# Kernel tuning notes

Measured on AMD Instinct MI355X. Metric: run time of the kernel, lower is better.

The kernel has to match this reference:

```python
import jax, jax.numpy as jnp
import numpy as np
import math

D_MODEL = 768
N_HEADS = 12
D_K = 64
D_V = 64
NEG = -1e9


def setup_inputs() -> dict:
    key = jax.random.key(0)
    ks = jax.random.split(key, 12)
    bz, L = 8, 1024
    q = jax.random.normal(ks[0], (bz, L, D_MODEL), dtype=jnp.float32)
    k = jax.random.normal(ks[1], (bz, L, D_MODEL), dtype=jnp.float32)
    v = jax.random.normal(ks[2], (bz, L, D_MODEL), dtype=jnp.float32)
    att_mask = jax.random.randint(ks[3], (bz, L), 0, 2).astype(bool)  # True = padded
    # Linear weights stored as [in, out] (torch stores [out, in]; math y = x @ W + b)
    std_qk = math.sqrt(2.0 / (D_MODEL + D_K))
    std_v = math.sqrt(2.0 / (D_MODEL + D_V))
    Wq = jax.random.normal(ks[4], (D_MODEL, D_K * N_HEADS), dtype=jnp.float32) * std_qk
    Wk = jax.random.normal(ks[5], (D_MODEL, D_K * N_HEADS), dtype=jnp.float32) * std_qk
    Wv = jax.random.normal(ks[6], (D_MODEL, D_V * N_HEADS), dtype=jnp.float32) * std_v
    xav = math.sqrt(2.0 / (D_V * N_HEADS + D_MODEL))
    Wo = jax.random.normal(ks[7], (D_V * N_HEADS, D_MODEL), dtype=jnp.float32) * xav
    bq = jnp.zeros((D_K * N_HEADS,), jnp.float32)
    bk = jnp.zeros((D_K * N_HEADS,), jnp.float32)
    bv = jnp.zeros((D_V * N_HEADS,), jnp.float32)
    bo = jnp.zeros((D_MODEL,), jnp.float32)
    gamma = jnp.ones((D_MODEL,), jnp.float32)
    beta = jnp.zeros((D_MODEL,), jnp.float32)
    return {"q": q, "k": k, "v": v, "att_mask": att_mask,
            "Wq": Wq, "bq": bq, "Wk": Wk, "bk": bk, "Wv": Wv, "bv": bv,
            "Wo": Wo, "bo": bo, "gamma": gamma, "beta": beta}


def reference(q, k, v, att_mask, Wq, bq, Wk, bk, Wv, bv, Wo, bo, gamma, beta):
    bz, Lq, _ = q.shape
    Lk = k.shape[1]
    scale = 1.0 / math.sqrt(D_K)
    residual = q
    # [bz, H, L, d]
    qf = (q @ Wq + bq).reshape(bz, Lq, N_HEADS, D_K).transpose(0, 2, 1, 3)
    kf = (k @ Wk + bk).reshape(bz, Lk, N_HEADS, D_K).transpose(0, 2, 1, 3)
    vf = (v @ Wv + bv).reshape(bz, Lk, N_HEADS, D_V).transpose(0, 2, 1, 3)
    scores = jnp.einsum('bhqd,bhkd->bhqk', qf, kf) * scale
    # padding mask: True positions set to -1e9 (masked_fill semantics)
    scores = jnp.where(att_mask[:, None, None, :], NEG, scores)
    iq = jnp.arange(Lq)[:, None]
    ik = jnp.arange(Lk)[None, :]
    fw = scores + jnp.where(ik < iq, NEG, 0.0).astype(scores.dtype)  # attend diag & above
    bw = scores + jnp.where(ik > iq, NEG, 0.0).astype(scores.dtype)  # attend diag & below
    a_fw = jax.nn.softmax(fw, axis=-1)
    a_bw = jax.nn.softmax(bw, axis=-1)
    att = jnp.einsum('bhqk,bhkd->bhqd', a_fw, vf) + jnp.einsum('bhqk,bhkd->bhqd', a_bw, vf)
    att = att.transpose(0, 2, 1, 3).reshape(bz, Lq, N_HEADS * D_V)
    mh = att @ Wo + bo
    x = residual + mh
    mu = jnp.mean(x, axis=-1, keepdims=True)
    var = jnp.mean(jnp.square(x - mu), axis=-1, keepdims=True)
    return (x - mu) / jnp.sqrt(var + 1e-6) * gamma + beta
```

## Files before the change

kernel.cpp:

```cpp
#include <hip/hip_runtime.h>
#include <hip/hip_bf16.h>

typedef unsigned short u16;
typedef unsigned int u32;
typedef unsigned long long u64;
typedef __attribute__((ext_vector_type(8))) short short8v;
typedef __attribute__((ext_vector_type(4))) float f32x4;

#define MFMA16(a,b,c) __builtin_amdgcn_mfma_f32_16x16x32_bf16(a,b,c,0,0,0)
#define NEGV -1e9f
#define MOFF 20.0f

__device__ __forceinline__ float b2f(u16 u){ return __uint_as_float(((u32)u)<<16); }
__device__ __forceinline__ u16 f2b(float f){
  __hip_bfloat16 h = __float2bfloat16(f);
  return __builtin_bit_cast(u16, h);
}
__device__ __forceinline__ u32 pk2(float a, float b){
  return (u32)f2b(a) | ((u32)f2b(b) << 16);
}

__global__ __launch_bounds__(256) void wcvt(
    const float* __restrict__ W0, const float* __restrict__ W1,
    const float* __restrict__ W2, const float* __restrict__ W3,
    u16* __restrict__ Wt)
{
  __shared__ u16 Tl[64*72];
  const int z = blockIdx.z;
  const float* W = z==0 ? W0 : z==1 ? W1 : z==2 ? W2 : W3;
  u16* Wo = Wt + (size_t)z * 768 * 768;
  const int t = threadIdx.x;
  const int n0 = blockIdx.x*64, k0 = blockIdx.y*64;
  const int r = t>>2, cs = (t&3)*16;
  {
    const float* src = W + (size_t)(k0+r)*768 + n0 + cs;
    float4 f0 = ((const float4*)src)[0];
    float4 f1 = ((const float4*)src)[1];
    float4 f2 = ((const float4*)src)[2];
    float4 f3 = ((const float4*)src)[3];
    uint4 o0 = { pk2(f0.x,f0.y), pk2(f0.z,f0.w), pk2(f1.x,f1.y), pk2(f1.z,f1.w) };
    uint4 o1 = { pk2(f2.x,f2.y), pk2(f2.z,f2.w), pk2(f3.x,f3.y), pk2(f3.z,f3.w) };
    *(uint4*)&Tl[r*72 + cs]     = o0;
    *(uint4*)&Tl[r*72 + cs + 8] = o1;
  }
  __syncthreads();
  {
    u16 v[16];
    #pragma unroll
    for (int j = 0; j < 16; ++j) v[j] = Tl[(cs+j)*72 + r];
    uint4 o0, o1;
    u32* p0 = (u32*)&o0; u32* p1 = (u32*)&o1;
    #pragma unroll
    for (int j = 0; j < 4; ++j) p0[j] = (u32)v[2*j] | ((u32)v[2*j+1]<<16);
    #pragma unroll
    for (int j = 0; j < 4; ++j) p1[j] = (u32)v[8+2*j] | ((u32)v[8+2*j+1]<<16);
    *(uint4*)(Wo + (size_t)(n0+r)*768 + k0 + cs)     = o0;
    *(uint4*)(Wo + (size_t)(n0+r)*768 + k0 + cs + 8) = o1;
  }
}

template<int ABF16, int OMODE>
__global__ __launch_bounds__(256) void gemm_mfma(
    const void* __restrict__ Av, const u16* __restrict__ Wt,
    const float* __restrict__ bias, float* __restrict__ outF,
    u16* __restrict__ outB)
{
  __shared__ u16 Al[128*40];
  __shared__ u16 Bl[128*40];
  const int t = threadIdx.x;
  const int lane = t & 63, wid = t >> 6;
  const int l15 = lane & 15, lg = lane >> 4;
  const int wm = wid >> 1, wn = wid & 1;

  const int id = blockIdx.x;
  const int xcd = id & 7, rr = id >> 3;
  const int nb = rr % 6, mb = (rr / 6) * 8 + xcd;
  const int n0 = nb * 128, m0 = mb * 128;

  f32x4 acc[4][4];
  #pragma unroll
  for (int mi = 0; mi < 4; ++mi)
    #pragma unroll
    for (int ni = 0; ni < 4; ++ni)
      acc[mi][ni] = (f32x4){0.f,0.f,0.f,0.f};

  const int arow = t >> 1, aseg = (t & 1) * 16;

  for (int k0 = 0; k0 < 768; k0 += 32) {
    __syncthreads();
    if (ABF16) {
      const u16* A = (const u16*)Av + (size_t)(m0 + arow) * 768 + k0 + aseg;
      uint4 a0 = ((const uint4*)A)[0];
      uint4 a1 = ((const uint4*)A)[1];
      *(uint4*)&Al[arow*40 + aseg]     = a0;
      *(uint4*)&Al[arow*40 + aseg + 8] = a1;
    } else {
      const float* A = (const float*)Av + (size_t)(m0 + arow) * 768 + k0 + aseg;
      float4 f0 = ((const float4*)A)[0];
      float4 f1 = ((const float4*)A)[1];
      float4 f2 = ((const float4*)A)[2];
      float4 f3 = ((const float4*)A)[3];
      uint4 o0 = { pk2(f0.x,f0.y), pk2(f0.z,f0.w), pk2(f1.x,f1.y), pk2(f1.z,f1.w) };
      uint4 o1 = { pk2(f2.x,f2.y), pk2(f2.z,f2.w), pk2(f3.x,f3.y), pk2(f3.z,f3.w) };
      *(uint4*)&Al[arow*40 + aseg]     = o0;
      *(uint4*)&Al[arow*40 + aseg + 8] = o1;
    }
    {
      const u16* B = Wt + (size_t)(n0 + arow) * 768 + k0 + aseg;
      uint4 b0 = ((const uint4*)B)[0];
      uint4 b1 = ((const uint4*)B)[1];
      *(uint4*)&Bl[arow*40 + aseg]     = b0;
      *(uint4*)&Bl[arow*40 + aseg + 8] = b1;
    }
    __syncthreads();
    short8v af[4], bf[4];
    #pragma unroll
    for (int mi = 0; mi < 4; ++mi)
      af[mi] = *(const short8v*)&Al[(wm*64 + mi*16 + l15)*40 + lg*8];
    #pragma unroll
    for (int ni = 0; ni < 4; ++ni)
      bf[ni] = *(const short8v*)&Bl[(wn*64 + ni*16 + l15)*40 + lg*8];
    #pragma unroll
    for (int mi = 0; mi < 4; ++mi)
      #pragma unroll
      for (int ni = 0; ni < 4; ++ni)
        acc[mi][ni] = MFMA16(af[mi], bf[ni], acc[mi][ni]);
  }

  #pragma unroll
  for (int mi = 0; mi < 4; ++mi)
  #pragma unroll
  for (int ni = 0; ni < 4; ++ni) {
    const int col  = n0 + wn*64 + ni*16 + l15;
    const int row0 = m0 + wm*64 + mi*16 + lg*4;
    const float bv = bias[col];
    if (OMODE == 0) {
      #pragma unroll
      for (int r = 0; r < 4; ++r)
        outF[(size_t)(row0 + r) * 768 + col] = acc[mi][ni][r] + bv;
    } else if (OMODE == 1) {
      const int h = col >> 6, d = col & 63;
      #pragma unroll
      for (int r = 0; r < 4; ++r) {
        const int row = row0 + r;
        const int bb = row >> 10, l = row & 1023;
        outB[(((size_t)(bb*12 + h))*1024 + l)*64 + d] = f2b(acc[mi][ni][r] + bv);
      }
    } else {
      const int h = col >> 6, d = col & 63;
      const int bb = row0 >> 10, l0 = row0 & 1023;
      const int pos = (l0 & ~63) + ((l0 >> 5) & 1) * 32
                    + ((l0 >> 2) & 3) * 8 + ((l0 >> 4) & 1) * 4;
      ushort4 pk;
      pk.x = f2b(acc[mi][ni][0] + bv);
      pk.y = f2b(acc[mi][ni][1] + bv);
      pk.z = f2b(acc[mi][ni][2] + bv);
      pk.w = f2b(acc[mi][ni][3] + bv);
      *(ushort4*)(outB + (((size_t)(bb*12 + h))*64 + d)*1024 + pos) = pk;
    }
  }
}

template<int R>
__device__ __forceinline__ void slow_fix(
    int side, int b, int bh, int rowg0, int lane, int l15, int lg,
    const u16* __restrict__ Vs, const int* __restrict__ mask,
    float* spb, f32x4 (&acc)[4], float (&L)[4])
{
  u64 bal = __ballot(l15 == 0 && L[R] == 0.f);
  while (bal) {
    const int pos = __ffsll((unsigned long long)bal) - 1;
    bal &= bal - 1;
    const int lgi = pos >> 4;
    const int q = rowg0 + lgi*4 + R;
    const u16* vp = Vs + ((size_t)bh*64 + lane)*1024;
    const int* mp = mask + b*1024;
    float vsum = 0.f, cnt = 0.f;
    for (int m0 = 0; m0 < 1024; m0 += 8) {
      uint4 vv = *(const uint4*)(vp + m0);
      const u16* ve = (const u16*)&vv;
      const int kb = (m0 & ~63) + ((m0 >> 5) & 1) * 32 + ((m0 >> 3) & 3) * 4;
      #pragma unroll
      for (int j = 0; j < 4; ++j) {
        const int k0 = kb + j, k1 = kb + 16 + j;
        const bool a0 = side ? (k0 <= q) : (k0 >= q);
        const bool a1 = side ? (k1 <= q) : (k1 >= q);
        const float w0 = a0 ? (mp[k0] ? 1.f : 0.f) : (mp[k0] ? 0.f : 1.f);
        const float w1 = a1 ? (mp[k1] ? 1.f : 0.f) : (mp[k1] ? 0.f : 1.f);
        vsum += w0 * b2f(ve[j]) + w1 * b2f(ve[4+j]);
        cnt  += w0 + w1;
      }
    }
    spb[lane] = vsum;
    if (lg == lgi) {
      #pragma unroll
      for (int fd = 0; fd < 4; ++fd)
        acc[fd][R] = spb[fd*16 + l15];
      L[R] = cnt;
    }
  }
}

__global__ __launch_bounds__(256, 4) void attn_mfma(
    const u16* __restrict__ Qf, const u16* __restrict__ Kf,
    const u16* __restrict__ Vs, const int* __restrict__ mask,
    u16* __restrict__ att)
{
  __shared__ u16 KV[2][2][4096];
  __shared__ float spb[4][64];

  const int t = threadIdx.x;
  const int lane = t & 63, wid = t >> 6;
  const int l15 = lane & 15, lg = lane >> 4;

  const int x = blockIdx.x;
  const int xcd = x & 7, rest = x >> 3;
  const int qt = rest & 15, bhh = rest >> 4;
  const int bh = (bhh << 3) | xcd;
  const int b = bh / 12, h = bh - b*12;
  const int rowg0 = qt*64 + wid*16;
  const int qglob = rowg0 + l15;

  short8v qb0, qb1;
  {
    const u16* Qp = Qf + ((size_t)bh*1024 + rowg0 + l15)*64 + lg*8;
    qb0 = *(const short8v*)(Qp);
    qb1 = *(const short8v*)(Qp + 32);
  }

  f32x4 accf[4], accb[4];
  #pragma unroll
  for (int i = 0; i < 4; ++i) { accf[i] = (f32x4){0,0,0,0}; accb[i] = (f32x4){0,0,0,0}; }
  float Lf = 0.f, Lb = 0.f;

  const u16* Kbh = Kf + (size_t)bh*1024*64;
  const u16* Vbh = Vs + (size_t)bh*64*1024;
  const int* mbp = mask + b*1024;

  const int srow = t >> 2;
  const int sc   = (t & 3) * 2;
  const int wo0  = srow*64 + ((sc     ^ (srow & 7)) * 8);
  const int wo1  = srow*64 + (((sc+1) ^ (srow & 7)) * 8);
  const size_t kgo = (size_t)srow*64   + sc*8;
  const size_t vgo = (size_t)srow*1024 + sc*8;

  uint4 kA = *(const uint4*)(Kbh + kgo);
  uint4 kB = *(const uint4*)(Kbh + kgo + 8);
  uint4 vA = *(const uint4*)(Vbh + vgo);
  uint4 vB = *(const uint4*)(Vbh + vgo + 8);
  *(uint4*)(&KV[0][0][wo0]) = kA;
  *(uint4*)(&KV[0][0][wo1]) = kB;
  *(uint4*)(&KV[0][1][wo0]) = vA;
  *(uint4*)(&KV[0][1][wo1]) = vB;
  __syncthreads();

  int buf = 0;
  for (int kt = 0; kt < 16; ++kt) {
    if (kt < 15) {
      kA = *(const uint4*)(Kbh + (size_t)(kt+1)*64*64 + kgo);
      kB = *(const uint4*)(Kbh + (size_t)(kt+1)*64*64 + kgo + 8);
      vA = *(const uint4*)(Vbh + (size_t)(kt+1)*64 + vgo);
      vB = *(const uint4*)(Vbh + (size_t)(kt+1)*64 + vgo + 8);
    }

    const u16* KB = KV[buf][0];
    const u16* VB = KV[buf][1];

    f32x4 sv[4];
    #pragma unroll
    for (int ni = 0; ni < 4; ++ni) {
      const int krow = ni*16 + l15;
      const int s0 = (lg ^ (l15 & 7)) * 8;
      short8v ka0 = *(const short8v*)(KB + krow*64 + s0);
      short8v ka1 = *(const short8v*)(KB + krow*64 + (s0 ^ 32));
      f32x4 z = (f32x4){0,0,0,0};
      z = MFMA16(ka0, qb0, z);
      z = MFMA16(ka1, qb1, z);
      int4 pm = *(const int4*)(mbp + kt*64 + ni*16 + lg*4);
      z[0] = pm.x ? NEGV : z[0]*0.125f;
      z[1] = pm.y ? NEGV : z[1]*0.125f;
      z[2] = pm.z ? NEGV : z[2]*0.125f;
      z[3] = pm.w ? NEGV : z[3]*0.125f;
      sv[ni] = z;
    }
    const bool dg = (kt == qt);

    #pragma unroll
    for (int side = 0; side < 2; ++side) {
      if (side == 0 && kt < qt) continue;
      if (side == 1 && kt > qt) continue;
      float p[4][4];
      float Ladd = 0.f;
      #pragma unroll
      for (int ni = 0; ni < 4; ++ni)
        #pragma unroll
        for (int r = 0; r < 4; ++r) {
          float arg = sv[ni][r];
          if (dg) {
            const int key = kt*64 + ni*16 + lg*4 + r;
            const bool msk = side ? (key > qglob) : (key < qglob);
            if (msk) arg += NEGV;
          }
          const float pe = __expf(arg - MOFF);
          p[ni][r] = pe;
          Ladd += pe;
        }
      if (side == 0) Lf += Ladd; else Lb += Ladd;
      f32x4* acc = side ? accb : accf;
      #pragma unroll
      for (int a = 0; a < 2; ++a) {
        uint4 pw;
        pw.x = pk2(p[2*a][0],   p[2*a][1]);
        pw.y = pk2(p[2*a][2],   p[2*a][3]);
        pw.z = pk2(p[2*a+1][0], p[2*a+1][1]);
        pw.w = pk2(p[2*a+1][2], p[2*a+1][3]);
        short8v pa = __builtin_bit_cast(short8v, pw);
        #pragma unroll
        for (int fd = 0; fd < 4; ++fd) {
          const int vrow = fd*16 + l15;
          const int vs2 = ((a*4 + lg) ^ (l15 & 7)) * 8;
          short8v vb = *(const short8v*)(VB + vrow*64 + vs2);
          acc[fd] = MFMA16(pa, vb, acc[fd]);
        }
      }
    }

    if (kt < 15) {
      *(uint4*)(&KV[buf^1][0][wo0]) = kA;
      *(uint4*)(&KV[buf^1][0][wo1]) = kB;
      *(uint4*)(&KV[buf^1][1][wo0]) = vA;
      *(uint4*)(&KV[buf^1][1][wo1]) = vB;
    }
    __syncthreads();
    buf ^= 1;
  }

  Lf += __shfl_xor(Lf, 16); Lf += __shfl_xor(Lf, 32);
  Lb += __shfl_xor(Lb, 16); Lb += __shfl_xor(Lb, 32);
  float Lfr[4], Lbr[4];
  #pragma unroll
  for (int r = 0; r < 4; ++r) {
    const int src = (lg << 4) | (lg*4 + r);
    Lfr[r] = __shfl(Lf, src);
    Lbr[r] = __shfl(Lb, src);
  }

  float* sp = spb[wid];
  slow_fix<0>(0, b, bh, rowg0, lane, l15, lg, Vs, mask, sp, accf, Lfr);
  slow_fix<1>(0, b, bh, rowg0, lane, l15, lg, Vs, mask, sp, accf, Lfr);
  slow_fix<2>(0, b, bh, rowg0, lane, l15, lg, Vs, mask, sp, accf, Lfr);
  slow_fix<3>(0, b, bh, rowg0, lane, l15, lg, Vs, mask, sp, accf, Lfr);
  slow_fix<0>(1, b, bh, rowg0, lane, l15, lg, Vs, mask, sp, accb, Lbr);
  slow_fix<1>(1, b, bh, rowg0, lane, l15, lg, Vs, mask, sp, accb, Lbr);
  slow_fix<2>(1, b, bh, rowg0, lane, l15, lg, Vs, mask, sp, accb, Lbr);
  slow_fix<3>(1, b, bh, rowg0, lane, l15, lg, Vs, mask, sp, accb, Lbr);

  float rf[4], rb[4];
  #pragma unroll
  for (int r = 0; r < 4; ++r) { rf[r] = 1.f/Lfr[r]; rb[r] = 1.f/Lbr[r]; }
  #pragma unroll
  for (int fd = 0; fd < 4; ++fd)
    #pragma unroll
    for (int r = 0; r < 4; ++r) {
      const float val = accf[fd][r]*rf[r] + accb[fd][r]*rb[r];
      att[((size_t)(b*1024 + rowg0 + lg*4 + r))*768 + h*64 + fd*16 + l15] = f2b(val);
    }
}

__global__ __launch_bounds__(256) void resid_ln(
    const float* __restrict__ qin, const float* __restrict__ proj,
    const float* __restrict__ gamma, const float* __restrict__ beta,
    float* __restrict__ out)
{
    __shared__ float red[4];
    const int row = blockIdx.x;
    const int t = threadIdx.x;
    const size_t base = (size_t)row * 768;

    float x0 = qin[base + t      ] + proj[base + t      ];
    float x1 = qin[base + t + 256] + proj[base + t + 256];
    float x2 = qin[base + t + 512] + proj[base + t + 512];

    float s = x0 + x1 + x2;
    #pragma unroll
    for (int m = 32; m >= 1; m >>= 1) s += __shfl_xor(s, m);
    if ((t & 63) == 0) red[t >> 6] = s;
    __syncthreads();
    float mu = (red[0] + red[1] + red[2] + red[3]) * (1.f / 768.f);

    float d0 = x0 - mu, d1 = x1 - mu, d2 = x2 - mu;
    float vs = d0 * d0 + d1 * d1 + d2 * d2;
    #pragma unroll
    for (int m = 32; m >= 1; m >>= 1) vs += __shfl_xor(vs, m);
    __syncthreads();
    if ((t & 63) == 0) red[t >> 6] = vs;
    __syncthreads();
    float var = (red[0] + red[1] + red[2] + red[3]) * (1.f / 768.f);
    float inv = rsqrtf(var + 1e-6f);

    out[base + t      ] = d0 * inv * gamma[t      ] + beta[t      ];
    out[base + t + 256] = d1 * inv * gamma[t + 256] + beta[t + 256];
    out[base + t + 512] = d2 * inv * gamma[t + 512] + beta[t + 512];
}

extern "C" void kernel_launch(void* const* d_in, const int* in_sizes, int n_in,
                              void* d_out, int out_size, void* d_ws, size_t ws_size,
                              hipStream_t stream)
{
    const float* q     = (const float*)d_in[0];
    const float* k     = (const float*)d_in[1];
    const float* v     = (const float*)d_in[2];
    const int*   mask  = (const int*)d_in[3];
    const float* Wq    = (const float*)d_in[4];
    const float* bq    = (const float*)d_in[5];
    const float* Wk    = (const float*)d_in[6];
    const float* bk    = (const float*)d_in[7];
    const float* Wv    = (const float*)d_in[8];
    const float* bv    = (const float*)d_in[9];
    const float* Wo    = (const float*)d_in[10];
    const float* bo    = (const float*)d_in[11];
    const float* gamma = (const float*)d_in[12];
    const float* beta  = (const float*)d_in[13];

    const size_t NE = (size_t)8 * 1024 * 768;
    const size_t WS = (size_t)768 * 768;
    u16* Qf  = (u16*)d_ws;
    u16* Kf  = Qf + NE;
    u16* Vs  = Kf + NE;
    u16* att = Vs + NE;
    u16* Wt  = att + NE;
    float* proj = (float*)Qf;

    dim3 blk(256);

    wcvt<<<dim3(12,12,4), blk, 0, stream>>>(Wq, Wk, Wv, Wo, Wt);

    gemm_mfma<0,1><<<384, blk, 0, stream>>>(q, Wt,        bq, nullptr, Qf);
    gemm_mfma<0,1><<<384, blk, 0, stream>>>(k, Wt + WS,   bk, nullptr, Kf);
    gemm_mfma<0,2><<<384, blk, 0, stream>>>(v, Wt + 2*WS, bv, nullptr, Vs);

    attn_mfma<<<1536, blk, 0, stream>>>(Qf, Kf, Vs, mask, att);

    gemm_mfma<1,0><<<384, blk, 0, stream>>>(att, Wt + 3*WS, bo, proj, nullptr);

    resid_ln<<<8192, blk, 0, stream>>>(q, proj, gamma, beta, (float*)d_out);
}
```

Before: 360.8 us.

## Merge QKV projection launches and process two query tiles per attention block

Combines the three Q/K/V projection GEMMs into one launch of 1152 blocks, so a single larger grid replaces three launches and their tail effects. The attention kernel now handles two 64-row query tiles per block (768 blocks instead of 1536), so each K/V tile staged in shared memory is reused by twice as many queries, halving K/V global and LDS staging traffic. V prefetch is moved later in the loop to keep register pressure down. The cost is more accumulators and registers per thread, which may lower occupancy under the existing launch bounds. Fewer blocks also leaves less parallelism to spread across the GPU.

```diff
diff --git a/kernel.cpp b/kernel.cpp
--- a/kernel.cpp
+++ b/kernel.cpp
@@ -59,11 +59,12 @@
   }
 }
 
-template<int ABF16, int OMODE>
-__global__ __launch_bounds__(256) void gemm_mfma(
-    const void* __restrict__ Av, const u16* __restrict__ Wt,
-    const float* __restrict__ bias, float* __restrict__ outF,
-    u16* __restrict__ outB)
+__global__ __launch_bounds__(256) void gemm_qkv(
+    const float* __restrict__ qi, const float* __restrict__ ki,
+    const float* __restrict__ vi, const u16* __restrict__ Wt,
+    const float* __restrict__ bq, const float* __restrict__ bk,
+    const float* __restrict__ bv,
+    u16* __restrict__ Qf, u16* __restrict__ Kf, u16* __restrict__ Vs)
 {
   __shared__ u16 Al[128*40];
   __shared__ u16 Bl[128*40];
@@ -73,6 +74,102 @@
   const int wm = wid >> 1, wn = wid & 1;
 
   const int id = blockIdx.x;
+  const int sub = id / 384;
+  const int rem = id - sub*384;
+  const float* A = sub==0 ? qi : sub==1 ? ki : vi;
+  const u16* W = Wt + (size_t)sub * 768 * 768;
+  const float* bias = sub==0 ? bq : sub==1 ? bk : bv;
+  u16* outB = sub==0 ? Qf : sub==1 ? Kf : Vs;
+
+  const int xcd = rem & 7, rr = rem >> 3;
+  const int nb = rr % 6, mb = (rr / 6) * 8 + xcd;
+  const int n0 = nb * 128, m0 = mb * 128;
+
+  f32x4 acc[4][4];
+  #pragma unroll
+  for (int mi = 0; mi < 4; ++mi)
+    #pragma unroll
+    for (int ni = 0; ni < 4; ++ni)
+      acc[mi][ni] = (f32x4){0.f,0.f,0.f,0.f};
+
+  const int arow = t >> 1, aseg = (t & 1) * 16;
+
+  for (int k0 = 0; k0 < 768; k0 += 32) {
+    __syncthreads();
+    {
+      const float* Ap = A + (size_t)(m0 + arow) * 768 + k0 + aseg;
+      float4 f0 = ((const float4*)Ap)[0];
+      float4 f1 = ((const float4*)Ap)[1];
+      float4 f2 = ((const float4*)Ap)[2];
+      float4 f3 = ((const float4*)Ap)[3];
+      uint4 o0 = { pk2(f0.x,f0.y), pk2(f0.z,f0.w), pk2(f1.x,f1.y), pk2(f1.z,f1.w) };
+      uint4 o1 = { pk2(f2.x,f2.y), pk2(f2.z,f2.w), pk2(f3.x,f3.y), pk2(f3.z,f3.w) };
+      *(uint4*)&Al[arow*40 + aseg]     = o0;
+      *(uint4*)&Al[arow*40 + aseg + 8] = o1;
+    }
+    {
+      const u16* B = W + (size_t)(n0 + arow) * 768 + k0 + aseg;
+      uint4 b0 = ((const uint4*)B)[0];
+      uint4 b1 = ((const uint4*)B)[1];
+      *(uint4*)&Bl[arow*40 + aseg]     = b0;
+      *(uint4*)&Bl[arow*40 + aseg + 8] = b1;
+    }
+    __syncthreads();
+    short8v af[4], bf[4];
+    #pragma unroll
+    for (int mi = 0; mi < 4; ++mi)
+      af[mi] = *(const short8v*)&Al[(wm*64 + mi*16 + l15)*40 + lg*8];
+    #pragma unroll
+    for (int ni = 0; ni < 4; ++ni)
+      bf[ni] = *(const short8v*)&Bl[(wn*64 + ni*16 + l15)*40 + lg*8];
+    #pragma unroll
+    for (int mi = 0; mi < 4; ++mi)
+      #pragma unroll
+      for (int ni = 0; ni < 4; ++ni)
+        acc[mi][ni] = MFMA16(af[mi], bf[ni], acc[mi][ni]);
+  }
+
+  #pragma unroll
+  for (int mi = 0; mi < 4; ++mi)
+  #pragma unroll
+  for (int ni = 0; ni < 4; ++ni) {
+    const int col  = n0 + wn*64 + ni*16 + l15;
+    const int row0 = m0 + wm*64 + mi*16 + lg*4;
+    const float bvv = bias[col];
+    const int h = col >> 6, d = col & 63;
+    if (sub < 2) {
+      #pragma unroll
+      for (int r = 0; r < 4; ++r) {
+        const int row = row0 + r;
+        const int bb = row >> 10, l = row & 1023;
+        outB[(((size_t)(bb*12 + h))*1024 + l)*64 + d] = f2b(acc[mi][ni][r] + bvv);
+      }
+    } else {
+      const int bb = row0 >> 10, l0 = row0 & 1023;
+      const int pos = (l0 & ~63) + ((l0 >> 5) & 1) * 32
+                    + ((l0 >> 2) & 3) * 8 + ((l0 >> 4) & 1) * 4;
+      ushort4 pk;
+      pk.x = f2b(acc[mi][ni][0] + bvv);
+      pk.y = f2b(acc[mi][ni][1] + bvv);
+      pk.z = f2b(acc[mi][ni][2] + bvv);
+      pk.w = f2b(acc[mi][ni][3] + bvv);
+      *(ushort4*)(outB + (((size_t)(bb*12 + h))*64 + d)*1024 + pos) = pk;
+    }
+  }
+}
+
+__global__ __launch_bounds__(256) void gemm_out(
+    const u16* __restrict__ Av, const u16* __restrict__ Wt,
+    const float* __restrict__ bias, float* __restrict__ outF)
+{
+  __shared__ u16 Al[128*40];
+  __shared__ u16 Bl[128*40];
+  const int t = threadIdx.x;
+  const int lane = t & 63, wid = t >> 6;
+  const int l15 = lane & 15, lg = lane >> 4;
+  const int wm = wid >> 1, wn = wid & 1;
+
+  const int id = blockIdx.x;
   const int xcd = id & 7, rr = id >> 3;
   const int nb = rr % 6, mb = (rr / 6) * 8 + xcd;
   const int n0 = nb * 128, m0 = mb * 128;
@@ -88,22 +185,12 @@
 
   for (int k0 = 0; k0 < 768; k0 += 32) {
     __syncthreads();
-    if (ABF16) {
-      const u16* A = (const u16*)Av + (size_t)(m0 + arow) * 768 + k0 + aseg;
+    {
+      const u16* A = Av + (size_t)(m0 + arow) * 768 + k0 + aseg;
       uint4 a0 = ((const uint4*)A)[0];
       uint4 a1 = ((const uint4*)A)[1];
       *(uint4*)&Al[arow*40 + aseg]     = a0;
       *(uint4*)&Al[arow*40 + aseg + 8] = a1;
-    } else {
-      const float* A = (const float*)Av + (size_t)(m0 + arow) * 768 + k0 + aseg;
-      float4 f0 = ((const float4*)A)[0];
-      float4 f1 = ((const float4*)A)[1];
-      float4 f2 = ((const float4*)A)[2];
-      float4 f3 = ((const float4*)A)[3];
-      uint4 o0 = { pk2(f0.x,f0.y), pk2(f0.z,f0.w), pk2(f1.x,f1.y), pk2(f1.z,f1.w) };
-      uint4 o1 = { pk2(f2.x,f2.y), pk2(f2.z,f2.w), pk2(f3.x,f3.y), pk2(f3.z,f3.w) };
-      *(uint4*)&Al[arow*40 + aseg]     = o0;
-      *(uint4*)&Al[arow*40 + aseg + 8] = o1;
     }
     {
       const u16* B = Wt + (size_t)(n0 + arow) * 768 + k0 + aseg;
@@ -133,31 +220,76 @@
   for (int ni = 0; ni < 4; ++ni) {
     const int col  = n0 + wn*64 + ni*16 + l15;
     const int row0 = m0 + wm*64 + mi*16 + lg*4;
-    const float bv = bias[col];
-    if (OMODE == 0) {
-      #pragma unroll
-      for (int r = 0; r < 4; ++r)
-        outF[(size_t)(row0 + r) * 768 + col] = acc[mi][ni][r] + bv;
-    } else if (OMODE == 1) {
-      const int h = col >> 6, d = col & 63;
-      #pragma unroll
-      for (int r = 0; r < 4; ++r) {
-        const int row = row0 + r;
-        const int bb = row >> 10, l = row & 1023;
-        outB[(((size_t)(bb*12 + h))*1024 + l)*64 + d] = f2b(acc[mi][ni][r] + bv);
+    const float bvv = bias[col];
+    #pragma unroll
+    for (int r = 0; r < 4; ++r)
+      outF[(size_t)(row0 + r) * 768 + col] = acc[mi][ni][r] + bvv;
+  }
+}
+
+__device__ __forceinline__ void qk_unit(
+    const u16* KB_, const short8v &q0, const short8v &q1,
+    const int* mbp, int kt, int l15, int lg, f32x4 (&sv)[4])
+{
+  #pragma unroll
+  for (int ni = 0; ni < 4; ++ni) {
+    const int krow = ni*16 + l15;
+    const int s0 = (lg ^ (l15 & 7)) * 8;
+    short8v ka0 = *(const short8v*)(KB_ + krow*64 + s0);
+    short8v ka1 = *(const short8v*)(KB_ + krow*64 + (s0 ^ 32));
+    f32x4 z = (f32x4){0,0,0,0};
+    z = MFMA16(ka0, q0, z);
+    z = MFMA16(ka1, q1, z);
+    int4 pm = *(const int4*)(mbp + kt*64 + ni*16 + lg*4);
+    z[0] = pm.x ? NEGV : z[0]*0.125f;
+    z[1] = pm.y ? NEGV : z[1]*0.125f;
+    z[2] = pm.z ? NEGV : z[2]*0.125f;
+    z[3] = pm.w ? NEGV : z[3]*0.125f;
+    sv[ni] = z;
+  }
+}
+
+__device__ __forceinline__ void su_unit(
+    const f32x4 (&sv)[4], f32x4 (&acc)[4], float &L,
+    int side, bool diag, int kt, int qg, int l15, int lg,
+    const u16* VB_)
+{
+  float Ladd = 0.f;
+  uint4 pw0, pw1;
+  u32* w0 = (u32*)&pw0; u32* w1 = (u32*)&pw1;
+  #pragma unroll
+  for (int ni = 0; ni < 4; ++ni) {
+    float pe[4];
+    #pragma unroll
+    for (int r = 0; r < 4; ++r) {
+      float arg = sv[ni][r];
+      if (diag) {
+        const int key = kt*64 + ni*16 + lg*4 + r;
+        const bool msk = side ? (key > qg) : (key < qg);
+        if (msk) arg += NEGV;
       }
-    } else {
-      const int h = col >> 6, d = col & 63;
-      const int bb = row0 >> 10, l0 = row0 & 1023;
-      const int pos = (l0 & ~63) + ((l0 >> 5) & 1) * 32
-                    + ((l0 >> 2) & 3) * 8 + ((l0 >> 4) & 1) * 4;
-      ushort4 pk;
-      pk.x = f2b(acc[mi][ni][0] + bv);
-      pk.y = f2b(acc[mi][ni][1] + bv);
-      pk.z = f2b(acc[mi][ni][2] + bv);
-      pk.w = f2b(acc[mi][ni][3] + bv);
-      *(ushort4*)(outB + (((size_t)(bb*12 + h))*64 + d)*1024 + pos) = pk;
-    }
+      pe[r] = __expf(arg - MOFF);
+      Ladd += pe[r];
+    }
+    const u32 lo = pk2(pe[0], pe[1]);
+    const u32 hi = pk2(pe[2], pe[3]);
+    if (ni == 0) { w0[0] = lo; w0[1] = hi; }
+    else if (ni == 1) { w0[2] = lo; w0[3] = hi; }
+    else if (ni == 2) { w1[0] = lo; w1[1] = hi; }
+    else { w1[2] = lo; w1[3] = hi; }
+  }
+  L += Ladd;
+  short8v pa0 = __builtin_bit_cast(short8v, pw0);
+  short8v pa1 = __builtin_bit_cast(short8v, pw1);
+  #pragma unroll
+  for (int fd = 0; fd < 4; ++fd) {
+    const int vrow = fd*16 + l15;
+    const int vs0 = ((lg)     ^ (l15 & 7)) * 8;
+    const int vs1 = ((4 + lg) ^ (l15 & 7)) * 8;
+    short8v vb0 = *(const short8v*)(VB_ + vrow*64 + vs0);
+    short8v vb1 = *(const short8v*)(VB_ + vrow*64 + vs1);
+    acc[fd] = MFMA16(pa0, vb0, acc[fd]);
+    acc[fd] = MFMA16(pa1, vb1, acc[fd]);
   }
 }
 
@@ -215,23 +347,36 @@
 
   const int x = blockIdx.x;
   const int xcd = x & 7, rest = x >> 3;
-  const int qt = rest & 15, bhh = rest >> 4;
-  const int bh = (bhh << 3) | xcd;
+  const int qj = rest & 7, bhh = rest >> 3;
+  const int bh = bhh*8 + xcd;
   const int b = bh / 12, h = bh - b*12;
-  const int rowg0 = qt*64 + wid*16;
-  const int qglob = rowg0 + l15;
-
-  short8v qb0, qb1;
+
+  const int row00 = qj*128 + wid*16;
+  const int row01 = row00 + 64;
+  const int qt0 = qj*2, qt1 = qj*2 + 1;
+  const int qg0 = row00 + l15, qg1 = row01 + l15;
+
+  short8v qb00, qb01, qb10, qb11;
   {
-    const u16* Qp = Qf + ((size_t)bh*1024 + rowg0 + l15)*64 + lg*8;
-    qb0 = *(const short8v*)(Qp);
-    qb1 = *(const short8v*)(Qp + 32);
-  }
-
-  f32x4 accf[4], accb[4];
-  #pragma unroll
-  for (int i = 0; i < 4; ++i) { accf[i] = (f32x4){0,0,0,0}; accb[i] = (f32x4){0,0,0,0}; }
-  float Lf = 0.f, Lb = 0.f;
+    const u16* Qp = Qf + ((size_t)bh*1024 + qg0)*64 + lg*8;
+    qb00 = *(const short8v*)(Qp);
+    qb01 = *(const short8v*)(Qp + 32);
+  }
+  {
+    const u16* Qp = Qf + ((size_t)bh*1024 + qg1)*64 + lg*8;
+    qb10 = *(const short8v*)(Qp);
+    qb11 = *(const short8v*)(Qp + 32);
+  }
+
+  f32x4 acc[2][2][4];
+  #pragma unroll
+  for (int u = 0; u < 2; ++u)
+    #pragma unroll
+    for (int s = 0; s < 2; ++s)
+      #pragma unroll
+      for (int fd = 0; fd < 4; ++fd)
+        acc[u][s][fd] = (f32x4){0,0,0,0};
+  float Lacc[2][2] = {{0.f,0.f},{0.f,0.f}};
 
   const u16* Kbh = Kf + (size_t)bh*1024*64;
   const u16* Vbh = Vs + (size_t)bh*64*1024;
@@ -244,90 +389,49 @@
   const size_t kgo = (size_t)srow*64   + sc*8;
   const size_t vgo = (size_t)srow*1024 + sc*8;
 
-  uint4 kA = *(const uint4*)(Kbh + kgo);
-  uint4 kB = *(const uint4*)(Kbh + kgo + 8);
-  uint4 vA = *(const uint4*)(Vbh + vgo);
-  uint4 vB = *(const uint4*)(Vbh + vgo + 8);
-  *(uint4*)(&KV[0][0][wo0]) = kA;
-  *(uint4*)(&KV[0][0][wo1]) = kB;
-  *(uint4*)(&KV[0][1][wo0]) = vA;
-  *(uint4*)(&KV[0][1][wo1]) = vB;
+  {
+    uint4 kA = *(const uint4*)(Kbh + kgo);
+    uint4 kB = *(const uint4*)(Kbh + kgo + 8);
+    uint4 vA = *(const uint4*)(Vbh + vgo);
+    uint4 vB = *(const uint4*)(Vbh + vgo + 8);
+    *(uint4*)(&KV[0][0][wo0]) = kA;
+    *(uint4*)(&KV[0][0][wo1]) = kB;
+    *(uint4*)(&KV[0][1][wo0]) = vA;
+    *(uint4*)(&KV[0][1][wo1]) = vB;
+  }
   __syncthreads();
 
   int buf = 0;
   for (int kt = 0; kt < 16; ++kt) {
+    uint4 kA, kB, vA, vB;
     if (kt < 15) {
       kA = *(const uint4*)(Kbh + (size_t)(kt+1)*64*64 + kgo);
       kB = *(const uint4*)(Kbh + (size_t)(kt+1)*64*64 + kgo + 8);
-      vA = *(const uint4*)(Vbh + (size_t)(kt+1)*64 + vgo);
-      vB = *(const uint4*)(Vbh + (size_t)(kt+1)*64 + vgo + 8);
-    }
-
-    const u16* KB = KV[buf][0];
-    const u16* VB = KV[buf][1];
-
-    f32x4 sv[4];
-    #pragma unroll
-    for (int ni = 0; ni < 4; ++ni) {
-      const int krow = ni*16 + l15;
-      const int s0 = (lg ^ (l15 & 7)) * 8;
-      short8v ka0 = *(const short8v*)(KB + krow*64 + s0);
-      short8v ka1 = *(const short8v*)(KB + krow*64 + (s0 ^ 32));
-      f32x4 z = (f32x4){0,0,0,0};
-      z = MFMA16(ka0, qb0, z);
-      z = MFMA16(ka1, qb1, z);
-      int4 pm = *(const int4*)(mbp + kt*64 + ni*16 + lg*4);
-      z[0] = pm.x ? NEGV : z[0]*0.125f;
-      z[1] = pm.y ? NEGV : z[1]*0.125f;
-      z[2] = pm.z ? NEGV : z[2]*0.125f;
-      z[3] = pm.w ? NEGV : z[3]*0.125f;
-      sv[ni] = z;
-    }
-    const bool dg = (kt == qt);
-
-    #pragma unroll
-    for (int side = 0; side < 2; ++side) {
-      if (side == 0 && kt < qt) continue;
-      if (side == 1 && kt > qt) continue;
-      float p[4][4];
-      float Ladd = 0.f;
-      #pragma unroll
-      for (int ni = 0; ni < 4; ++ni)
-        #pragma unroll
-        for (int r = 0; r < 4; ++r) {
-          float arg = sv[ni][r];
-          if (dg) {
-            const int key = kt*64 + ni*16 + lg*4 + r;
-            const bool msk = side ? (key > qglob) : (key < qglob);
-            if (msk) arg += NEGV;
-          }
-          const float pe = __expf(arg - MOFF);
-          p[ni][r] = pe;
-          Ladd += pe;
-        }
-      if (side == 0) Lf += Ladd; else Lb += Ladd;
-      f32x4* acc = side ? accb : accf;
-      #pragma unroll
-      for (int a = 0; a < 2; ++a) {
-        uint4 pw;
-        pw.x = pk2(p[2*a][0],   p[2*a][1]);
-        pw.y = pk2(p[2*a][2],   p[2*a][3]);
-        pw.z = pk2(p[2*a+1][0], p[2*a+1][1]);
-        pw.w = pk2(p[2*a+1][2], p[2*a+1][3]);
-        short8v pa = __builtin_bit_cast(short8v, pw);
-        #pragma unroll
-        for (int fd = 0; fd < 4; ++fd) {
-          const int vrow = fd*16 + l15;
-          const int vs2 = ((a*4 + lg) ^ (l15 & 7)) * 8;
-          short8v vb = *(const short8v*)(VB + vrow*64 + vs2);
-          acc[fd] = MFMA16(pa, vb, acc[fd]);
-        }
-      }
-    }
+    }
+    const u16* KB_ = KV[buf][0];
+    const u16* VB_ = KV[buf][1];
+
+    f32x4 sv0[4];
+    qk_unit(KB_, qb00, qb01, mbp, kt, l15, lg, sv0);
 
     if (kt < 15) {
       *(uint4*)(&KV[buf^1][0][wo0]) = kA;
       *(uint4*)(&KV[buf^1][0][wo1]) = kB;
+      vA = *(const uint4*)(Vbh + (size_t)(kt+1)*64 + vgo);
+      vB = *(const uint4*)(Vbh + (size_t)(kt+1)*64 + vgo + 8);
+    }
+
+    if (kt >= qt0) su_unit(sv0, acc[0][0], Lacc[0][0], 0, kt==qt0, kt, qg0, l15, lg, VB_);
+    if (kt <= qt0) su_unit(sv0, acc[0][1], Lacc[0][1], 1, kt==qt0, kt, qg0, l15, lg, VB_);
+
+    {
+      f32x4 sv1[4];
+      qk_unit(KB_, qb10, qb11, mbp, kt, l15, lg, sv1);
+      if (kt >= qt1) su_unit(sv1, acc[1][0], Lacc[1][0], 0, kt==qt1, kt, qg1, l15, lg, VB_);
+      if (kt <= qt1) su_unit(sv1, acc[1][1], Lacc[1][1], 1, kt==qt1, kt, qg1, l15, lg, VB_);
+    }
+
+    if (kt < 15) {
       *(uint4*)(&KV[buf^1][1][wo0]) = vA;
       *(uint4*)(&KV[buf^1][1][wo1]) = vB;
     }
@@ -335,36 +439,52 @@
     buf ^= 1;
   }
 
-  Lf += __shfl_xor(Lf, 16); Lf += __shfl_xor(Lf, 32);
-  Lb += __shfl_xor(Lb, 16); Lb += __shfl_xor(Lb, 32);
-  float Lfr[4], Lbr[4];
-  #pragma unroll
-  for (int r = 0; r < 4; ++r) {
-    const int src = (lg << 4) | (lg*4 + r);
-    Lfr[r] = __shfl(Lf, src);
-    Lbr[r] = __shfl(Lb, src);
+  float Lfr[2][4], Lbr[2][4];
+  #pragma unroll
+  for (int u = 0; u < 2; ++u) {
+    float lf = Lacc[u][0], lb = Lacc[u][1];
+    lf += __shfl_xor(lf, 16); lf += __shfl_xor(lf, 32);
+    lb += __shfl_xor(lb, 16); lb += __shfl_xor(lb, 32);
+    #pragma unroll
+    for (int r = 0; r < 4; ++r) {
+      const int src = (lg << 4) | (lg*4 + r);
+      Lfr[u][r] = __shfl(lf, src);
+      Lbr[u][r] = __shfl(lb, src);
+    }
   }
 
   float* sp = spb[wid];
-  slow_fix<0>(0, b, bh, rowg0, lane, l15, lg, Vs, mask, sp, accf, Lfr);
-  slow_fix<1>(0, b, bh, rowg0, lane, l15, lg, Vs, mask, sp, accf, Lfr);
-  slow_fix<2>(0, b, bh, rowg0, lane, l15, lg, Vs, mask, sp, accf, Lfr);
-  slow_fix<3>(0, b, bh, rowg0, lane, l15, lg, Vs, mask, sp, accf, Lfr);
-  slow_fix<0>(1, b, bh, rowg0, lane, l15, lg, Vs, mask, sp, accb, Lbr);
-  slow_fix<1>(1, b, bh, rowg0, lane, l15, lg, Vs, mask, sp, accb, Lbr);
-  slow_fix<2>(1, b, bh, rowg0, lane, l15, lg, Vs, mask, sp, accb, Lbr);
-  slow_fix<3>(1, b, bh, rowg0, lane, l15, lg, Vs, mask, sp, accb, Lbr);
-
-  float rf[4], rb[4];
-  #pragma unroll
-  for (int r = 0; r < 4; ++r) { rf[r] = 1.f/Lfr[r]; rb[r] = 1.f/Lbr[r]; }
-  #pragma unroll
-  for (int fd = 0; fd < 4; ++fd)
-    #pragma unroll
-    for (int r = 0; r < 4; ++r) {
-      const float val = accf[fd][r]*rf[r] + accb[fd][r]*rb[r];
-      att[((size_t)(b*1024 + rowg0 + lg*4 + r))*768 + h*64 + fd*16 + l15] = f2b(val);
-    }
+  slow_fix<0>(0, b, bh, row00, lane, l15, lg, Vs, mask, sp, acc[0][0], Lfr[0]);
+  slow_fix<1>(0, b, bh, row00, lane, l15, lg, Vs, mask, sp, acc[0][0], Lfr[0]);
+  slow_fix<2>(0, b, bh, row00, lane, l15, lg, Vs, mask, sp, acc[0][0], Lfr[0]);
+  slow_fix<3>(0, b, bh, row00, lane, l15, lg, Vs, mask, sp, acc[0][0], Lfr[0]);
+  slow_fix<0>(1, b, bh, row00, lane, l15, lg, Vs, mask, sp, acc[0][1], Lbr[0]);
+  slow_fix<1>(1, b, bh, row00, lane, l15, lg, Vs, mask, sp, acc[0][1], Lbr[0]);
+  slow_fix<2>(1, b, bh, row00, lane, l15, lg, Vs, mask, sp, acc[0][1], Lbr[0]);
+  slow_fix<3>(1, b, bh, row00, lane, l15, lg, Vs, mask, sp, acc[0][1], Lbr[0]);
+  slow_fix<0>(0, b, bh, row01, lane, l15, lg, Vs, mask, sp, acc[1][0], Lfr[1]);
+  slow_fix<1>(0, b, bh, row01, lane, l15, lg, Vs, mask, sp, acc[1][0], Lfr[1]);
+  slow_fix<2>(0, b, bh, row01, lane, l15, lg, Vs, mask, sp, acc[1][0], Lfr[1]);
+  slow_fix<3>(0, b, bh, row01, lane, l15, lg, Vs, mask, sp, acc[1][0], Lfr[1]);
+  slow_fix<0>(1, b, bh, row01, lane, l15, lg, Vs, mask, sp, acc[1][1], Lbr[1]);
+  slow_fix<1>(1, b, bh, row01, lane, l15, lg, Vs, mask, sp, acc[1][1], Lbr[1]);
+  slow_fix<2>(1, b, bh, row01, lane, l15, lg, Vs, mask, sp, acc[1][1], Lbr[1]);
+  slow_fix<3>(1, b, bh, row01, lane, l15, lg, Vs, mask, sp, acc[1][1], Lbr[1]);
+
+  #pragma unroll
+  for (int u = 0; u < 2; ++u) {
+    const int r0 = (u == 0) ? row00 : row01;
+    float rf[4], rb[4];
+    #pragma unroll
+    for (int r = 0; r < 4; ++r) { rf[r] = 1.f/Lfr[u][r]; rb[r] = 1.f/Lbr[u][r]; }
+    #pragma unroll
+    for (int fd = 0; fd < 4; ++fd)
+      #pragma unroll
+      for (int r = 0; r < 4; ++r) {
+        const float val = acc[u][0][fd][r]*rf[r] + acc[u][1][fd][r]*rb[r];
+        att[((size_t)(b*1024 + r0 + lg*4 + r))*768 + h*64 + fd*16 + l15] = f2b(val);
+      }
+  }
 }
 
 __global__ __launch_bounds__(256) void resid_ln(
@@ -435,13 +555,11 @@
 
     wcvt<<<dim3(12,12,4), blk, 0, stream>>>(Wq, Wk, Wv, Wo, Wt);
 
-    gemm_mfma<0,1><<<384, blk, 0, stream>>>(q, Wt,        bq, nullptr, Qf);
-    gemm_mfma<0,1><<<384, blk, 0, stream>>>(k, Wt + WS,   bk, nullptr, Kf);
-    gemm_mfma<0,2><<<384, blk, 0, stream>>>(v, Wt + 2*WS, bv, nullptr, Vs);
-
-    attn_mfma<<<1536, blk, 0, stream>>>(Qf, Kf, Vs, mask, att);
-
-    gemm_mfma<1,0><<<384, blk, 0, stream>>>(att, Wt + 3*WS, bo, proj, nullptr);
+    gemm_qkv<<<1152, blk, 0, stream>>>(q, k, v, Wt, bq, bk, bv, Qf, Kf, Vs);
+
+    attn_mfma<<<768, blk, 0, stream>>>(Qf, Kf, Vs, mask, att);
+
+    gemm_out<<<384, blk, 0, stream>>>(att, Wt + 3*WS, bo, proj);
 
     resid_ln<<<8192, blk, 0, stream>>>(q, proj, gamma, beta, (float*)d_out);
 }
```

New measurement: 369.5 us. +2.4%, slower.
